# Performance work log

Hardware: AMD Instinct MI355X
Metric: run time of the kernel (lower is better)

The kernel has to match this reference:

```python
import jax, jax.numpy as jnp
import numpy as np

MODEL_DIM = 1024
NUM_HEADS = 16
D_K = MODEL_DIM // NUM_HEADS  # 64
MAX_SEQ_LEN = 4096


def _xavier(key, shape):
    fan_in, fan_out = shape[1], shape[0]
    limit = np.sqrt(6.0 / (fan_in + fan_out)).astype(np.float32)
    return jax.random.uniform(key, shape, jnp.float32, -limit, limit)


def setup_inputs() -> dict:
    key = jax.random.key(0)
    ks = jax.random.split(key, 6)
    x = jax.random.normal(ks[0], (2, 2048, MODEL_DIM), jnp.float32)
    wq = _xavier(ks[1], (MODEL_DIM, MODEL_DIM))
    wk = _xavier(ks[2], (MODEL_DIM, MODEL_DIM))
    wv = _xavier(ks[3], (MODEL_DIM, MODEL_DIM))
    wo = _xavier(ks[4], (MODEL_DIM, MODEL_DIM))
    bq = jnp.zeros((MODEL_DIM,), jnp.float32)
    bk = jnp.zeros((MODEL_DIM,), jnp.float32)
    bv = jnp.zeros((MODEL_DIM,), jnp.float32)
    bo = jnp.zeros((MODEL_DIM,), jnp.float32)
    # precomputed rotary tables (cos/sin of position * theta^(-2i/d))
    half = D_K // 2
    theta = jnp.power(10000.0, jnp.arange(half, dtype=jnp.float32) * (-2.0 / D_K))
    angles = jnp.arange(MAX_SEQ_LEN, dtype=jnp.float32)[:, None] * theta[None, :]
    rot_cos = jnp.cos(angles)  # [max_seq_len, d_k//2]
    rot_sin = jnp.sin(angles)
    return {"x": x, "wq": wq, "bq": bq, "wk": wk, "bk": bk,
            "wv": wv, "bv": bv, "wo": wo, "bo": bo,
            "rot_cos": rot_cos, "rot_sin": rot_sin}


def reference(x, wq, bq, wk, bk, wv, bv, wo, bo, rot_cos, rot_sin):
    b, t, m = x.shape
    h, d = NUM_HEADS, m // NUM_HEADS
    # NOTE: original uses .view (reshape), NOT transpose, to split heads.
    q = (x @ wq.T + bq).reshape(b, h, t, d)
    k = (x @ wk.T + bk).reshape(b, h, t, d)
    v = (x @ wv.T + bv).reshape(b, h, t, d)
    # Faithful to original: rotation matrix indexed by scalar position == seq_len,
    # so every token uses the SAME rotation angle (position t).
    c = rot_cos[t]  # [d//2]
    s = rot_sin[t]

    def rope(u):
        ur = u.reshape(b, h, t, d // 2, 2)
        re, im = ur[..., 0], ur[..., 1]
        return jnp.stack([re * c - im * s, re * s + im * c], axis=-1).reshape(b, h, t, d)

    q, k = rope(q), rope(k)
    scores = jnp.einsum('bhqd,bhkd->bhqk', q, k) / np.float32(np.sqrt(d))
    p = jax.nn.softmax(scores, axis=-1)  # mask='none', dropout=0.0
    o = jnp.einsum('bhqk,bhkd->bhqd', p, v)
    o = o.transpose(0, 2, 1, 3).reshape(b, t, m)  # 'b h t d -> b t (h d)'
    return o @ wo.T + bo
```

## Files before the change

### kernel.cpp

```cpp
#include <hip/hip_runtime.h>
#include <hip/hip_bf16.h>
#include <stdint.h>


typedef __attribute__((ext_vector_type(8))) short bf16x8;
typedef bf16x8 __attribute__((may_alias)) bf16x8_a;
typedef __attribute__((ext_vector_type(4))) float f32x4;
typedef f32x4 __attribute__((may_alias)) f32x4_a;
typedef __attribute__((ext_vector_type(2))) unsigned int u32x2;
typedef u32x2 __attribute__((may_alias)) u32x2_a;

__device__ inline unsigned short f2b(float f) {
  union { float f; unsigned int u; } x; x.f = f;
  unsigned int r = x.u + 0x7fffu + ((x.u >> 16) & 1u);
  return (unsigned short)(r >> 16);
}

__device__ inline unsigned cvtpk_bf16(float lo, float hi) {
  unsigned r;
  asm("v_cvt_pk_bf16_f32 %0, %1, %2" : "=v"(r) : "v"(lo), "v"(hi));
  return r;
}

__global__ __launch_bounds__(256) void cvt_all(
    const float* __restrict__ x,
    const float* __restrict__ w0, const float* __restrict__ w1,
    const float* __restrict__ w2, const float* __restrict__ w3,
    unsigned short* __restrict__ xb,
    unsigned short* __restrict__ o0, unsigned short* __restrict__ o1,
    unsigned short* __restrict__ o2, unsigned short* __restrict__ o3) {
  int bid = blockIdx.x;
  const float* in; unsigned short* out; int i;
  if (bid < 4096) { in = x; out = xb; i = bid * 256 + threadIdx.x; }
  else {
    int w = (bid - 4096) >> 10;
    in = (w == 0) ? w0 : (w == 1) ? w1 : (w == 2) ? w2 : w3;
    out = (w == 0) ? o0 : (w == 1) ? o1 : (w == 2) ? o2 : o3;
    i = ((bid - 4096) & 1023) * 256 + threadIdx.x;
  }
  float4 v = reinterpret_cast<const float4*>(in)[i];
  ushort4 o;
  o.x = f2b(v.x); o.y = f2b(v.y); o.z = f2b(v.z); o.w = f2b(v.w);
  reinterpret_cast<ushort4*>(out)[i] = o;
}

template<int MODE>
__global__ __launch_bounds__(256) void gemm_bt(
    const unsigned short* __restrict__ A,
    const unsigned short* __restrict__ W0, const unsigned short* __restrict__ W1,
    const unsigned short* __restrict__ W2,
    const float* __restrict__ b0, const float* __restrict__ b1, const float* __restrict__ b2,
    unsigned short* __restrict__ o0, unsigned short* __restrict__ o1,
    unsigned short* __restrict__ o2,
    float* __restrict__ of, int M, int N, int K)
{
  const int tid = threadIdx.x;
  const int lane = tid & 63;
  const int wid = tid >> 6;
  const int q4 = lane >> 4;
  const int l15 = lane & 15;
  const int wr = wid >> 1, wc = wid & 1;

  const unsigned short* W = W0; const float* bias = b0; unsigned short* ob = o0;
  if (MODE == 0) {
    if (blockIdx.z == 1) { W = W1; bias = b1; ob = o1; }
    else if (blockIdx.z == 2) { W = W2; bias = b2; ob = o2; }
  }
  const bool vsw = (MODE == 0) && (blockIdx.z == 2);

  __shared__ __align__(16) unsigned short sA[2][128 * 64];
  __shared__ __align__(16) unsigned short sB[2][64 * 64];
  char* sAc = (char*)sA;
  char* sBc = (char*)sB;

  f32x4 acc[4][2];
#pragma unroll
  for (int i = 0; i < 4; ++i)
#pragma unroll
    for (int j = 0; j < 2; ++j) acc[i][j] = (f32x4){0.f, 0.f, 0.f, 0.f};

  const size_t rowA0 = (size_t)blockIdx.x * 128;
  const size_t rowB0 = (size_t)blockIdx.y * 64;
  const int wt = (int)(blockIdx.y >> 1);
  const int xt = (int)(blockIdx.x * 2 + (blockIdx.y & 1));

  const unsigned short* srcA0 = vsw ? (W + (size_t)wt * 128 * K) : (A + rowA0 * K);
  const unsigned short* srcB0 = vsw ? (A + (size_t)xt * 64 * K) : (W + rowB0 * K);

  auto stage = [&](int bs, int k0) {
#pragma unroll
    for (int it = 0; it < 4; ++it) {
      int Loff = it * 4096 + wid * 1024;
      int L = Loff + lane * 16;
      int row = L >> 7;
      int csrc = ((L >> 4) & 7) ^ (row & 7);
      const unsigned short* ga = srcA0 + (size_t)row * K + k0 + csrc * 8;
      __builtin_amdgcn_global_load_lds((const __attribute__((address_space(1))) void*)ga,
                                       (__attribute__((address_space(3))) void*)(sAc + bs * 16384 + Loff),
                                       16, 0, 0);
    }
#pragma unroll
    for (int it = 0; it < 2; ++it) {
      int Loff = it * 4096 + wid * 1024;
      int L = Loff + lane * 16;
      int row = L >> 7;
      int csrc = ((L >> 4) & 7) ^ (row & 7);
      const unsigned short* gw = srcB0 + (size_t)row * K + k0 + csrc * 8;
      __builtin_amdgcn_global_load_lds((const __attribute__((address_space(1))) void*)gw,
                                       (__attribute__((address_space(3))) void*)(sBc + bs * 8192 + Loff),
                                       16, 0, 0);
    }
  };

  stage(0, 0);

  const int NT = K >> 6;
  for (int t = 0; t < NT; ++t) {
    const int cur = t & 1;
    __syncthreads();
    if (t + 1 < NT) stage(cur ^ 1, (t + 1) * 64);

#pragma unroll
    for (int ks = 0; ks < 2; ++ks) {
      bf16x8 af[4], bfr[2];
#pragma unroll
      for (int f = 0; f < 4; ++f) {
        int ra = wr * 64 + f * 16 + l15;
        af[f] = *(const bf16x8_a*)(sAc + cur * 16384 + ra * 128 +
                                   ((ks * 64 + q4 * 16) ^ ((ra & 7) << 4)));
      }
#pragma unroll
      for (int f = 0; f < 2; ++f) {
        int rb = wc * 32 + f * 16 + l15;
        bfr[f] = *(const bf16x8_a*)(sBc + cur * 8192 + rb * 128 +
                                    ((ks * 64 + q4 * 16) ^ ((rb & 7) << 4)));
      }
      __builtin_amdgcn_s_setprio(1);
#pragma unroll
      for (int i = 0; i < 4; ++i)
#pragma unroll
        for (int j = 0; j < 2; ++j)
          acc[i][j] = __builtin_amdgcn_mfma_f32_16x16x32_bf16(af[i], bfr[j], acc[i][j], 0, 0, 0);
      __builtin_amdgcn_s_setprio(0);
    }
  }

  if (MODE == 0 && blockIdx.z == 2) {
    const int bb = xt >> 1;
    const int sbase = (xt & 1) * 64;
#pragma unroll
    for (int i = 0; i < 4; ++i) {
      const int nb = wt * 128 + wr * 64 + i * 16 + q4 * 4;
#pragma unroll
      for (int j = 0; j < 2; ++j) {
        const int srow = sbase + wc * 32 + j * 16 + l15;
#pragma unroll
        for (int r = 0; r < 4; ++r) {
          const int n = nb + r;
          ob[(size_t)bb * 131072 + (size_t)(n & 63) * 2048 +
             (size_t)(n >> 6) * 128 + srow] = f2b(acc[i][j][r] + bias[n]);
        }
      }
    }
  } else {
#pragma unroll
    for (int i = 0; i < 4; ++i) {
      int row = (int)rowA0 + wr * 64 + i * 16 + q4 * 4;
#pragma unroll
      for (int j = 0; j < 2; ++j) {
        int col = (int)rowB0 + wc * 32 + j * 16 + l15;
        float bv = bias[col];
        if (MODE == 0 && blockIdx.z == 1) {
#pragma unroll
          for (int r = 0; r < 4; ++r) {
            size_t a = (size_t)((row + r) >> 7) * 131072 +
                       (size_t)(((col >> 6) << 7) + ((row + r) & 127)) * 64 + (col & 63);
            ob[a] = f2b(acc[i][j][r] + bv);
          }
        } else {
#pragma unroll
          for (int r = 0; r < 4; ++r) {
            float v = acc[i][j][r] + bv;
            if (MODE == 0) ob[(size_t)(row + r) * N + col] = f2b(v * 0.18033688f);
            else           of[(size_t)(row + r) * N + col] = v;
          }
        }
      }
    }
  }
}

__global__ __launch_bounds__(512, 4) void attn_kernel(
    const unsigned short* __restrict__ Qg,
    const unsigned short* __restrict__ Kg,
    const unsigned short* __restrict__ VTg,
    unsigned short* __restrict__ ctx)
{
  const int tid = threadIdx.x;
  const int lane = tid & 63;
  const int wid = tid >> 6;
  const int half = wid >> 2;
  const int wq = wid & 3;
  const int q4 = lane >> 4;
  const int l15 = lane & 15;

  const int bid = blockIdx.x;
  const int bh = (bid & 7) * 4 + ((bid >> 3) >> 4);
  const int qt = (bid >> 3) & 15;
  const int b = bh >> 4, h = bh & 15;
  const size_t base = (size_t)bh * 131072;
  const unsigned short* Qh = Qg + base;
  const unsigned short* Kh = Kg + base;
  const unsigned short* VTh = VTg + base;
  const int q0 = qt * 128;
  const int kvbase = half * 1024;

  __shared__ __align__(16) char smem[49152];
  char* sKc = smem;
  char* sVc = smem + 16384;
  char* sPw = smem + 32768 + wid * 2048;

  bf16x8 qf[2][2];
#pragma unroll
  for (int s = 0; s < 2; ++s)
#pragma unroll
    for (int ks = 0; ks < 2; ++ks)
      qf[s][ks] = *(const bf16x8*)(Qh + (size_t)(q0 + wq * 32 + s * 16 + l15) * 64 + ks * 32 + q4 * 8);

  const int u = tid & 255;
  const int rK = u >> 3;
  const int cK = ((u & 7) ^ (rK & 7)) * 8;
  const unsigned short* gK = Kh + (size_t)(kvbase + rK) * 64 + cK;
  const int rV = u >> 3;
  const int cV = (u & 7) ^ (rV & 7);
  const int dV = rV * 2 + (cV >> 2);
  const unsigned short* gV = VTh + (size_t)dV * 2048 + kvbase + (cV & 3) * 8;

  auto stage = [&](int bs, int t) {
    char* dK = sKc + half * 8192 + bs * 4096 + wq * 1024;
    char* dV_ = sVc + half * 8192 + bs * 4096 + wq * 1024;
    __builtin_amdgcn_global_load_lds(
        (const __attribute__((address_space(1))) void*)(gK + (size_t)t * 2048),
        (__attribute__((address_space(3))) void*)dK, 16, 0, 0);
    __builtin_amdgcn_global_load_lds(
        (const __attribute__((address_space(1))) void*)(gV + t * 32),
        (__attribute__((address_space(3))) void*)dV_, 16, 0, 0);
  };

  const int vp_chunk = (((l15 & 1) * 4 + q4) ^ ((l15 >> 1) & 7)) * 16;
  const int vp_row = (l15 >> 1) * 128;

  f32x4 oacc[2][4];
#pragma unroll
  for (int s = 0; s < 2; ++s)
#pragma unroll
    for (int fn = 0; fn < 4; ++fn) oacc[s][fn] = (f32x4){0.f, 0.f, 0.f, 0.f};
  float m_run[2] = {-INFINITY, -INFINITY};
  float l_run[2] = {0.f, 0.f};

  stage(0, 0);

  for (int t = 0; t < 32; ++t) {
    const int cur = t & 1;
    __syncthreads();
    if (t < 31) stage(cur ^ 1, t + 1);

    char* kbuf = sKc + half * 8192 + cur * 4096;
    char* vbuf = sVc + half * 8192 + cur * 4096;

    f32x4 sc[2][2];
#pragma unroll
    for (int s = 0; s < 2; ++s)
#pragma unroll
      for (int fm = 0; fm < 2; ++fm) sc[s][fm] = (f32x4){0.f, 0.f, 0.f, 0.f};
    __builtin_amdgcn_s_setprio(1);
#pragma unroll
    for (int ks = 0; ks < 2; ++ks) {
#pragma unroll
      for (int fm = 0; fm < 2; ++fm) {
        const int rk = fm * 16 + l15;
        bf16x8_a kf = *(const bf16x8_a*)(kbuf + rk * 128 +
                                         ((ks * 64 + q4 * 16) ^ ((rk & 7) << 4)));
        sc[0][fm] = __builtin_amdgcn_mfma_f32_16x16x32_bf16(kf, qf[0][ks], sc[0][fm], 0, 0, 0);
        sc[1][fm] = __builtin_amdgcn_mfma_f32_16x16x32_bf16(kf, qf[1][ks], sc[1][fm], 0, 0, 0);
      }
    }
    __builtin_amdgcn_s_setprio(0);

#pragma unroll
    for (int s = 0; s < 2; ++s) {
      float mx = fmaxf(fmaxf(fmaxf(sc[s][0][0], sc[s][0][1]), fmaxf(sc[s][0][2], sc[s][0][3])),
                       fmaxf(fmaxf(sc[s][1][0], sc[s][1][1]), fmaxf(sc[s][1][2], sc[s][1][3])));
      mx = fmaxf(mx, __shfl_xor(mx, 16));
      mx = fmaxf(mx, __shfl_xor(mx, 32));
      if (!__all(mx <= m_run[s] + 11.54f)) {
        const float mnew = fmaxf(m_run[s], mx);
        const float sc_o = __builtin_amdgcn_exp2f(m_run[s] - mnew);
        l_run[s] *= sc_o;
        m_run[s] = mnew;
#pragma unroll
        for (int r = 0; r < 4; ++r) {
          const float so = __shfl(sc_o, (lane & 48) | (q4 * 4 + r));
#pragma unroll
          for (int fn = 0; fn < 4; ++fn) oacc[s][fn][r] *= so;
        }
      }
      float rs = 0.f;
#pragma unroll
      for (int fm = 0; fm < 2; ++fm)
#pragma unroll
        for (int r = 0; r < 4; ++r) {
          sc[s][fm][r] = __builtin_amdgcn_exp2f(sc[s][fm][r] - m_run[s]);
          rs += sc[s][fm][r];
        }
      rs += __shfl_xor(rs, 16);
      rs += __shfl_xor(rs, 32);
      l_run[s] += rs;

      char* rowp = sPw + (s * 8 + (l15 >> 1)) * 128;
      const int wbase = ((l15 & 1) * 4 + (q4 >> 1)) ^ ((l15 >> 1) & 7);
#pragma unroll
      for (int fm = 0; fm < 2; ++fm) {
        u32x2 pk;
        pk[0] = cvtpk_bf16(sc[s][fm][0], sc[s][fm][1]);
        pk[1] = cvtpk_bf16(sc[s][fm][2], sc[s][fm][3]);
        *(u32x2_a*)(rowp + ((wbase ^ (fm * 2)) << 4) + (q4 & 1) * 8) = pk;
      }
    }
    asm volatile("s_waitcnt lgkmcnt(0)" ::: "memory");
    __builtin_amdgcn_sched_barrier(0);

    bf16x8 pf[2];
#pragma unroll
    for (int s = 0; s < 2; ++s)
      pf[s] = *(const bf16x8_a*)(sPw + s * 1024 + vp_row + vp_chunk);
    __builtin_amdgcn_s_setprio(1);
#pragma unroll
    for (int fn = 0; fn < 4; ++fn) {
      bf16x8_a vf = *(const bf16x8_a*)(vbuf + fn * 1024 + vp_row + vp_chunk);
      oacc[0][fn] = __builtin_amdgcn_mfma_f32_16x16x32_bf16(pf[0], vf, oacc[0][fn], 0, 0, 0);
      oacc[1][fn] = __builtin_amdgcn_mfma_f32_16x16x32_bf16(pf[1], vf, oacc[1][fn], 0, 0, 0);
    }
    __builtin_amdgcn_s_setprio(0);
  }

  __syncthreads();
  if (half == 1) {
    char* mb = smem + wq * 8192;
#pragma unroll
    for (int s = 0; s < 2; ++s)
#pragma unroll
      for (int fn = 0; fn < 4; ++fn)
        *(f32x4_a*)(mb + (((s * 4 + fn) * 64) + lane) * 16) = oacc[s][fn];
    if (q4 == 0) {
#pragma unroll
      for (int s = 0; s < 2; ++s)
        *(float2*)(smem + 32768 + ((wq * 2 + s) * 16 + l15) * 8) =
            make_float2(m_run[s], l_run[s]);
    }
  }
  __syncthreads();
  if (half == 0) {
    char* mb = smem + wq * 8192;
#pragma unroll
    for (int s = 0; s < 2; ++s) {
      float2 ml = *(const float2*)(smem + 32768 + ((wq * 2 + s) * 16 + l15) * 8);
      const float mm = fmaxf(m_run[s], ml.x);
      const float w1 = __builtin_amdgcn_exp2f(m_run[s] - mm);
      const float w2 = __builtin_amdgcn_exp2f(ml.x - mm);
      const float li = 1.0f / (l_run[s] * w1 + ml.y * w2);
#pragma unroll
      for (int r = 0; r < 4; ++r) {
        const int src = (lane & 48) | (q4 * 4 + r);
        const float w1b = __shfl(w1, src);
        const float w2b = __shfl(w2, src);
        const float lib = __shfl(li, src);
        const int trow = q0 + wq * 32 + s * 16 + q4 * 4 + r;
        const size_t ro = ((size_t)b * 2048 + trow) * 1024 + h * 64;
#pragma unroll
        for (int fn = 0; fn < 4; ++fn) {
          f32x4 o2 = *(const f32x4_a*)(mb + (((s * 4 + fn) * 64) + lane) * 16);
          ctx[ro + fn * 16 + l15] = f2b((oacc[s][fn][r] * w1b + o2[r] * w2b) * lib);
        }
      }
    }
  }
}

extern "C" void kernel_launch(void* const* d_in, const int* in_sizes, int n_in,
                              void* d_out, int out_size, void* d_ws, size_t ws_size,
                              hipStream_t stream) {
  const float* x  = (const float*)d_in[0];
  const float* wq = (const float*)d_in[1];
  const float* bq = (const float*)d_in[2];
  const float* wk = (const float*)d_in[3];
  const float* bk = (const float*)d_in[4];
  const float* wv = (const float*)d_in[5];
  const float* bv = (const float*)d_in[6];
  const float* wo = (const float*)d_in[7];
  const float* bo = (const float*)d_in[8];

  char* ws = (char*)d_ws;
  unsigned short* xb  = (unsigned short*)(ws);
  unsigned short* wqb = (unsigned short*)(ws + 8388608);
  unsigned short* wkb = (unsigned short*)(ws + 10485760);
  unsigned short* wvb = (unsigned short*)(ws + 12582912);
  unsigned short* wob = (unsigned short*)(ws + 14680064);
  unsigned short* Qb  = (unsigned short*)(ws + 16777216);
  unsigned short* Kb  = (unsigned short*)(ws + 25165824);
  unsigned short* VTb = (unsigned short*)(ws + 33554432);
  unsigned short* ctx = xb;

  cvt_all<<<8192, 256, 0, stream>>>(x, wq, wk, wv, wo, xb, wqb, wkb, wvb, wob);

  gemm_bt<0><<<dim3(32, 16, 3), 256, 0, stream>>>(
      xb, wqb, wkb, wvb, bq, bk, bv, Qb, Kb, VTb, nullptr, 4096, 1024, 1024);

  attn_kernel<<<dim3(512), dim3(512), 0, stream>>>(Qb, Kb, VTb, ctx);

  gemm_bt<1><<<dim3(32, 16, 1), 256, 0, stream>>>(
      ctx, wob, nullptr, nullptr, bo, nullptr, nullptr, nullptr, nullptr, nullptr,
      (float*)d_out, 4096, 1024, 1024);
}
```

Before: 119.1 us.

## Halve attention query tile to 64 rows and double grid size

Each attention block now covers 64 query rows instead of 128, with one 16-row MFMA strip per wave instead of two. The grid doubles to 1024 blocks, shared memory drops to 40KB and the launch bounds ask for 8 waves per SIMD. The goal is more blocks and higher occupancy on the 256-CU part so latency is better hidden. In exchange, every K/V tile is loaded twice as often per query, and each K/V fragment read from LDS feeds only one MFMA instead of two.

After: 127.9 us. 1.07x slower.

```diff
diff --git a/kernel.cpp b/kernel.cpp
--- a/kernel.cpp
+++ b/kernel.cpp
@@ -190,7 +190,7 @@
   }
 }
 
-__global__ __launch_bounds__(512, 4) void attn_kernel(
+__global__ __launch_bounds__(512, 8) void attn_kernel(
     const unsigned short* __restrict__ Qg,
     const unsigned short* __restrict__ Kg,
     const unsigned short* __restrict__ VTg,
@@ -205,27 +205,26 @@
   const int l15 = lane & 15;
 
   const int bid = blockIdx.x;
-  const int bh = (bid & 7) * 4 + ((bid >> 3) >> 4);
-  const int qt = (bid >> 3) & 15;
+  const int r7 = bid >> 3;
+  const int bh = (bid & 7) * 4 + (r7 >> 5);
+  const int qt = r7 & 31;
   const int b = bh >> 4, h = bh & 15;
   const size_t base = (size_t)bh * 131072;
   const unsigned short* Qh = Qg + base;
   const unsigned short* Kh = Kg + base;
   const unsigned short* VTh = VTg + base;
-  const int q0 = qt * 128;
+  const int q0 = qt * 64;
   const int kvbase = half * 1024;
 
-  __shared__ __align__(16) char smem[49152];
+  __shared__ __align__(16) char smem[40960];
   char* sKc = smem;
   char* sVc = smem + 16384;
-  char* sPw = smem + 32768 + wid * 2048;
-
-  bf16x8 qf[2][2];
-#pragma unroll
-  for (int s = 0; s < 2; ++s)
-#pragma unroll
-    for (int ks = 0; ks < 2; ++ks)
-      qf[s][ks] = *(const bf16x8*)(Qh + (size_t)(q0 + wq * 32 + s * 16 + l15) * 64 + ks * 32 + q4 * 8);
+  char* sPw = smem + 32768 + wid * 1024;
+
+  bf16x8 qf[2];
+#pragma unroll
+  for (int ks = 0; ks < 2; ++ks)
+    qf[ks] = *(const bf16x8*)(Qh + (size_t)(q0 + wq * 16 + l15) * 64 + ks * 32 + q4 * 8);
 
   const int u = tid & 255;
   const int rK = u >> 3;
@@ -250,13 +249,10 @@
   const int vp_chunk = (((l15 & 1) * 4 + q4) ^ ((l15 >> 1) & 7)) * 16;
   const int vp_row = (l15 >> 1) * 128;
 
-  f32x4 oacc[2][4];
-#pragma unroll
-  for (int s = 0; s < 2; ++s)
-#pragma unroll
-    for (int fn = 0; fn < 4; ++fn) oacc[s][fn] = (f32x4){0.f, 0.f, 0.f, 0.f};
-  float m_run[2] = {-INFINITY, -INFINITY};
-  float l_run[2] = {0.f, 0.f};
+  f32x4 oacc[4];
+#pragma unroll
+  for (int fn = 0; fn < 4; ++fn) oacc[fn] = (f32x4){0.f, 0.f, 0.f, 0.f};
+  float m_run = -INFINITY, l_run = 0.f;
 
   stage(0, 0);
 
@@ -268,11 +264,9 @@
     char* kbuf = sKc + half * 8192 + cur * 4096;
     char* vbuf = sVc + half * 8192 + cur * 4096;
 
-    f32x4 sc[2][2];
-#pragma unroll
-    for (int s = 0; s < 2; ++s)
-#pragma unroll
-      for (int fm = 0; fm < 2; ++fm) sc[s][fm] = (f32x4){0.f, 0.f, 0.f, 0.f};
+    f32x4 sc[2];
+#pragma unroll
+    for (int fm = 0; fm < 2; ++fm) sc[fm] = (f32x4){0.f, 0.f, 0.f, 0.f};
     __builtin_amdgcn_s_setprio(1);
 #pragma unroll
     for (int ks = 0; ks < 2; ++ks) {
@@ -281,107 +275,92 @@
         const int rk = fm * 16 + l15;
         bf16x8_a kf = *(const bf16x8_a*)(kbuf + rk * 128 +
                                          ((ks * 64 + q4 * 16) ^ ((rk & 7) << 4)));
-        sc[0][fm] = __builtin_amdgcn_mfma_f32_16x16x32_bf16(kf, qf[0][ks], sc[0][fm], 0, 0, 0);
-        sc[1][fm] = __builtin_amdgcn_mfma_f32_16x16x32_bf16(kf, qf[1][ks], sc[1][fm], 0, 0, 0);
+        sc[fm] = __builtin_amdgcn_mfma_f32_16x16x32_bf16(kf, qf[ks], sc[fm], 0, 0, 0);
       }
     }
     __builtin_amdgcn_s_setprio(0);
 
-#pragma unroll
-    for (int s = 0; s < 2; ++s) {
-      float mx = fmaxf(fmaxf(fmaxf(sc[s][0][0], sc[s][0][1]), fmaxf(sc[s][0][2], sc[s][0][3])),
-                       fmaxf(fmaxf(sc[s][1][0], sc[s][1][1]), fmaxf(sc[s][1][2], sc[s][1][3])));
-      mx = fmaxf(mx, __shfl_xor(mx, 16));
-      mx = fmaxf(mx, __shfl_xor(mx, 32));
-      if (!__all(mx <= m_run[s] + 11.54f)) {
-        const float mnew = fmaxf(m_run[s], mx);
-        const float sc_o = __builtin_amdgcn_exp2f(m_run[s] - mnew);
-        l_run[s] *= sc_o;
-        m_run[s] = mnew;
-#pragma unroll
-        for (int r = 0; r < 4; ++r) {
-          const float so = __shfl(sc_o, (lane & 48) | (q4 * 4 + r));
-#pragma unroll
-          for (int fn = 0; fn < 4; ++fn) oacc[s][fn][r] *= so;
-        }
-      }
-      float rs = 0.f;
-#pragma unroll
-      for (int fm = 0; fm < 2; ++fm)
-#pragma unroll
-        for (int r = 0; r < 4; ++r) {
-          sc[s][fm][r] = __builtin_amdgcn_exp2f(sc[s][fm][r] - m_run[s]);
-          rs += sc[s][fm][r];
-        }
-      rs += __shfl_xor(rs, 16);
-      rs += __shfl_xor(rs, 32);
-      l_run[s] += rs;
-
-      char* rowp = sPw + (s * 8 + (l15 >> 1)) * 128;
+    float mx = fmaxf(fmaxf(fmaxf(sc[0][0], sc[0][1]), fmaxf(sc[0][2], sc[0][3])),
+                     fmaxf(fmaxf(sc[1][0], sc[1][1]), fmaxf(sc[1][2], sc[1][3])));
+    mx = fmaxf(mx, __shfl_xor(mx, 16));
+    mx = fmaxf(mx, __shfl_xor(mx, 32));
+    if (!__all(mx <= m_run + 11.54f)) {
+      const float mnew = fmaxf(m_run, mx);
+      const float sc_o = __builtin_amdgcn_exp2f(m_run - mnew);
+      l_run *= sc_o;
+      m_run = mnew;
+#pragma unroll
+      for (int r = 0; r < 4; ++r) {
+        const float so = __shfl(sc_o, (lane & 48) | (q4 * 4 + r));
+#pragma unroll
+        for (int fn = 0; fn < 4; ++fn) oacc[fn][r] *= so;
+      }
+    }
+    float rs = 0.f;
+#pragma unroll
+    for (int fm = 0; fm < 2; ++fm)
+#pragma unroll
+      for (int r = 0; r < 4; ++r) {
+        sc[fm][r] = __builtin_amdgcn_exp2f(sc[fm][r] - m_run);
+        rs += sc[fm][r];
+      }
+    rs += __shfl_xor(rs, 16);
+    rs += __shfl_xor(rs, 32);
+    l_run += rs;
+
+    {
+      char* rowp = sPw + (l15 >> 1) * 128;
       const int wbase = ((l15 & 1) * 4 + (q4 >> 1)) ^ ((l15 >> 1) & 7);
 #pragma unroll
       for (int fm = 0; fm < 2; ++fm) {
         u32x2 pk;
-        pk[0] = cvtpk_bf16(sc[s][fm][0], sc[s][fm][1]);
-        pk[1] = cvtpk_bf16(sc[s][fm][2], sc[s][fm][3]);
+        pk[0] = cvtpk_bf16(sc[fm][0], sc[fm][1]);
+        pk[1] = cvtpk_bf16(sc[fm][2], sc[fm][3]);
         *(u32x2_a*)(rowp + ((wbase ^ (fm * 2)) << 4) + (q4 & 1) * 8) = pk;
       }
     }
     asm volatile("s_waitcnt lgkmcnt(0)" ::: "memory");
     __builtin_amdgcn_sched_barrier(0);
 
-    bf16x8 pf[2];
-#pragma unroll
-    for (int s = 0; s < 2; ++s)
-      pf[s] = *(const bf16x8_a*)(sPw + s * 1024 + vp_row + vp_chunk);
+    bf16x8 pf = *(const bf16x8_a*)(sPw + vp_row + vp_chunk);
     __builtin_amdgcn_s_setprio(1);
 #pragma unroll
     for (int fn = 0; fn < 4; ++fn) {
       bf16x8_a vf = *(const bf16x8_a*)(vbuf + fn * 1024 + vp_row + vp_chunk);
-      oacc[0][fn] = __builtin_amdgcn_mfma_f32_16x16x32_bf16(pf[0], vf, oacc[0][fn], 0, 0, 0);
-      oacc[1][fn] = __builtin_amdgcn_mfma_f32_16x16x32_bf16(pf[1], vf, oacc[1][fn], 0, 0, 0);
+      oacc[fn] = __builtin_amdgcn_mfma_f32_16x16x32_bf16(pf, vf, oacc[fn], 0, 0, 0);
     }
     __builtin_amdgcn_s_setprio(0);
   }
 
   __syncthreads();
   if (half == 1) {
-    char* mb = smem + wq * 8192;
-#pragma unroll
-    for (int s = 0; s < 2; ++s)
-#pragma unroll
-      for (int fn = 0; fn < 4; ++fn)
-        *(f32x4_a*)(mb + (((s * 4 + fn) * 64) + lane) * 16) = oacc[s][fn];
-    if (q4 == 0) {
-#pragma unroll
-      for (int s = 0; s < 2; ++s)
-        *(float2*)(smem + 32768 + ((wq * 2 + s) * 16 + l15) * 8) =
-            make_float2(m_run[s], l_run[s]);
-    }
+    char* mb = smem + wq * 4096;
+#pragma unroll
+    for (int fn = 0; fn < 4; ++fn)
+      *(f32x4_a*)(mb + (fn * 64 + lane) * 16) = oacc[fn];
+    if (q4 == 0)
+      *(float2*)(smem + 16384 + (wq * 16 + l15) * 8) = make_float2(m_run, l_run);
   }
   __syncthreads();
   if (half == 0) {
-    char* mb = smem + wq * 8192;
-#pragma unroll
-    for (int s = 0; s < 2; ++s) {
-      float2 ml = *(const float2*)(smem + 32768 + ((wq * 2 + s) * 16 + l15) * 8);
-      const float mm = fmaxf(m_run[s], ml.x);
-      const float w1 = __builtin_amdgcn_exp2f(m_run[s] - mm);
-      const float w2 = __builtin_amdgcn_exp2f(ml.x - mm);
-      const float li = 1.0f / (l_run[s] * w1 + ml.y * w2);
-#pragma unroll
-      for (int r = 0; r < 4; ++r) {
-        const int src = (lane & 48) | (q4 * 4 + r);
-        const float w1b = __shfl(w1, src);
-        const float w2b = __shfl(w2, src);
-        const float lib = __shfl(li, src);
-        const int trow = q0 + wq * 32 + s * 16 + q4 * 4 + r;
-        const size_t ro = ((size_t)b * 2048 + trow) * 1024 + h * 64;
-#pragma unroll
-        for (int fn = 0; fn < 4; ++fn) {
-          f32x4 o2 = *(const f32x4_a*)(mb + (((s * 4 + fn) * 64) + lane) * 16);
-          ctx[ro + fn * 16 + l15] = f2b((oacc[s][fn][r] * w1b + o2[r] * w2b) * lib);
-        }
+    char* mb = smem + wq * 4096;
+    float2 ml = *(const float2*)(smem + 16384 + (wq * 16 + l15) * 8);
+    const float mm = fmaxf(m_run, ml.x);
+    const float w1 = __builtin_amdgcn_exp2f(m_run - mm);
+    const float w2 = __builtin_amdgcn_exp2f(ml.x - mm);
+    const float li = 1.0f / (l_run * w1 + ml.y * w2);
+#pragma unroll
+    for (int r = 0; r < 4; ++r) {
+      const int src = (lane & 48) | (q4 * 4 + r);
+      const float w1b = __shfl(w1, src);
+      const float w2b = __shfl(w2, src);
+      const float lib = __shfl(li, src);
+      const int trow = q0 + wq * 16 + q4 * 4 + r;
+      const size_t ro = ((size_t)b * 2048 + trow) * 1024 + h * 64;
+#pragma unroll
+      for (int fn = 0; fn < 4; ++fn) {
+        f32x4 o2 = *(const f32x4_a*)(mb + (fn * 64 + lane) * 16);
+        ctx[ro + fn * 16 + l15] = f2b((oacc[fn][r] * w1b + o2[r] * w2b) * lib);
       }
     }
   }
@@ -416,7 +395,7 @@
   gemm_bt<0><<<dim3(32, 16, 3), 256, 0, stream>>>(
       xb, wqb, wkb, wvb, bq, bk, bv, Qb, Kb, VTb, nullptr, 4096, 1024, 1024);
 
-  attn_kernel<<<dim3(512), dim3(512), 0, stream>>>(Qb, Kb, VTb, ctx);
+  attn_kernel<<<dim3(1024), dim3(512), 0, stream>>>(Qb, Kb, VTb, ctx);
 
   gemm_bt<1><<<dim3(32, 16, 1), 256, 0, stream>>>(
       ctx, wob, nullptr, nullptr, bo, nullptr, nullptr, nullptr, nullptr, nullptr,
```
